# Performance work log

Measured on AMD Instinct MI355X. Metric: run time of the kernel, lower is better.

## Reference

```python
import jax, jax.numpy as jnp
import numpy as np

D = 512
H = 8
DH = D // H
FF = 2 * D
EPS = 1e-5


def _layernorm(x, g, b):
    mu = jnp.mean(x, axis=-1, keepdims=True)
    var = jnp.mean(jnp.square(x - mu), axis=-1, keepdims=True)
    return (x - mu) * jax.lax.rsqrt(var + EPS) * g + b


def setup_inputs() -> dict:
    key = jax.random.key(0)
    ks = jax.random.split(key, 8)
    s = 0.02
    x = jax.random.normal(ks[0], (1, 4096, D), dtype=jnp.float32)
    w_qkv = jax.random.normal(ks[1], (D, 3 * D), dtype=jnp.float32) * s
    b_qkv = jnp.zeros((3 * D,), jnp.float32)
    w_out = jax.random.normal(ks[2], (D, D), dtype=jnp.float32) * s
    b_out = jnp.zeros((D,), jnp.float32)
    w_ff1 = jax.random.normal(ks[3], (D, FF), dtype=jnp.float32) * s
    b_ff1 = jnp.zeros((FF,), jnp.float32)
    w_ff2 = jax.random.normal(ks[4], (FF, D), dtype=jnp.float32) * s
    b_ff2 = jnp.zeros((D,), jnp.float32)
    g1 = jnp.ones((D,), jnp.float32)
    bt1 = jnp.zeros((D,), jnp.float32)
    g2 = jnp.ones((D,), jnp.float32)
    bt2 = jnp.zeros((D,), jnp.float32)
    return {"x": x, "w_qkv": w_qkv, "b_qkv": b_qkv, "w_out": w_out, "b_out": b_out,
            "w_ff1": w_ff1, "b_ff1": b_ff1, "w_ff2": w_ff2, "b_ff2": b_ff2,
            "g1": g1, "bt1": bt1, "g2": g2, "bt2": bt2}


def reference(x, w_qkv, b_qkv, w_out, b_out, w_ff1, b_ff1, w_ff2, b_ff2, g1, bt1, g2, bt2):
    B, S, _ = x.shape
    h = _layernorm(x, g1, bt1)
    qkv = h @ w_qkv + b_qkv                      # [B,S,3D]
    qkv = qkv.reshape(B, S, 3, H, DH)
    q, k, v = qkv[:, :, 0], qkv[:, :, 1], qkv[:, :, 2]   # [B,S,H,DH]
    scores = jnp.einsum('bqhd,bkhd->bhqk', q, k) / np.sqrt(DH).astype(np.float32)
    causal = jnp.tril(jnp.ones((S, S), dtype=bool))
    scores = jnp.where(causal, scores, -jnp.inf)
    attn = jax.nn.softmax(scores, axis=-1)
    out = jnp.einsum('bhqk,bkhd->bqhd', attn, v).reshape(B, S, D)
    x = x + out @ w_out + b_out
    h2 = _layernorm(x, g2, bt2)
    ff = jax.nn.gelu(h2 @ w_ff1 + b_ff1, approximate=False) @ w_ff2 + b_ff2
    return x + ff
```

## Files before the change

kernel.cpp:

```cpp
#include <hip/hip_runtime.h>
#include <math.h>

#define D 512
#define H 8
#define DH 64
#define S 4096
#define FF 1024

typedef __attribute__((ext_vector_type(8))) short bf16x8;
typedef __attribute__((ext_vector_type(4))) float f32x4;
typedef __attribute__((ext_vector_type(16))) float f32x16;

__device__ __forceinline__ unsigned short f2bf(float f) {
    union { float f; unsigned u; } c; c.f = f;
    unsigned r = (c.u + 0x7fff + ((c.u >> 16) & 1)) >> 16;
    return (unsigned short)r;
}
__device__ __forceinline__ float bf2f(unsigned short u) {
    union { unsigned u; float f; } c; c.u = ((unsigned)u) << 16;
    return c.f;
}

__device__ __forceinline__ void gl_lds16(const void* g, void* l) {
    __builtin_amdgcn_global_load_lds(
        (const __attribute__((address_space(1))) void*)g,
        (__attribute__((address_space(3))) void*)l, 16, 0, 0);
}

__global__ __launch_bounds__(256) void transpose_all(const float* __restrict__ wqkv,
                                                     const float* __restrict__ wout,
                                                     const float* __restrict__ wff1,
                                                     const float* __restrict__ wff2,
                                                     unsigned short* __restrict__ oqkv,
                                                     unsigned short* __restrict__ oout,
                                                     unsigned short* __restrict__ off1,
                                                     unsigned short* __restrict__ off2) {
    __shared__ unsigned short tile[32][33];
    int id = blockIdx.x;
    const float* src; unsigned short* dst; int K, N, lid;
    if (id < 768)       { src = wqkv; dst = oqkv; K = 512;  N = 1536; lid = id; }
    else if (id < 1024) { src = wout; dst = oout; K = 512;  N = 512;  lid = id - 768; }
    else if (id < 1536) { src = wff1; dst = off1; K = 512;  N = 1024; lid = id - 1024; }
    else                { src = wff2; dst = off2; K = 1024; N = 512;  lid = id - 1536; }
    int nb = N / 32;
    int n0 = (lid % nb) * 32, k0 = (lid / nb) * 32;
    int tx = threadIdx.x & 31, ty = threadIdx.x >> 5;
#pragma unroll
    for (int i = 0; i < 32; i += 8)
        tile[ty + i][tx] = f2bf(src[(size_t)(k0 + ty + i) * N + n0 + tx]);
    __syncthreads();
#pragma unroll
    for (int i = 0; i < 32; i += 8)
        dst[(size_t)(n0 + ty + i) * K + k0 + tx] = tile[tx][ty + i];
}

__global__ __launch_bounds__(256) void transpose_v(const unsigned short* __restrict__ qkv,
                                                   unsigned short* __restrict__ vT) {
    __shared__ unsigned short tile[32][33];
    int s0 = blockIdx.x * 32, d0 = blockIdx.y * 32;
    int tx = threadIdx.x & 31, ty = threadIdx.x >> 5;
#pragma unroll
    for (int i = 0; i < 32; i += 8)
        tile[ty + i][tx] = qkv[(size_t)(s0 + ty + i) * (3 * D) + 2 * D + d0 + tx];
    __syncthreads();
#pragma unroll
    for (int i = 0; i < 32; i += 8)
        vT[(size_t)(d0 + ty + i) * S + s0 + tx] = tile[tx][ty + i];
}

__global__ __launch_bounds__(256) void ln_kernel(const float* __restrict__ x,
                                                 const float* __restrict__ g,
                                                 const float* __restrict__ bta,
                                                 unsigned short* __restrict__ out) {
    int row = blockIdx.x, tid = threadIdx.x;
    const float* xr = x + (size_t)row * D;
    float2 v = *(const float2*)(xr + tid * 2);
    float s = v.x + v.y;
    float sq = v.x * v.x + v.y * v.y;
#pragma unroll
    for (int m = 1; m < 64; m <<= 1) { s += __shfl_xor(s, m); sq += __shfl_xor(sq, m); }
    __shared__ float red[8];
    int wave = tid >> 6, lane = tid & 63;
    if (lane == 0) { red[wave] = s; red[4 + wave] = sq; }
    __syncthreads();
    s = red[0] + red[1] + red[2] + red[3];
    sq = red[4] + red[5] + red[6] + red[7];
    float mu = s * (1.f / D);
    float var = sq * (1.f / D) - mu * mu;
    float rstd = rsqrtf(var + 1e-5f);
    int i = tid * 2;
    float2 gg = *(const float2*)(g + i);
    float2 bb = *(const float2*)(bta + i);
    out[(size_t)row * D + i]     = f2bf((v.x - mu) * rstd * gg.x + bb.x);
    out[(size_t)row * D + i + 1] = f2bf((v.y - mu) * rstd * gg.y + bb.y);
}

enum { EPI_BF16 = 0, EPI_RESID_F32 = 1, EPI_GELU_BF16 = 2 };

template <int EPI, int WMI>
__global__ __launch_bounds__(256, WMI == 4 ? 2 : 3)
void gemm3_kernel(const unsigned short* __restrict__ A,
                  const unsigned short* __restrict__ BT,
                  const float* __restrict__ bias,
                  const float* __restrict__ resid,
                  void* __restrict__ out,
                  int M, int N, int K) {
    constexpr int BM = 32 * WMI;
    constexpr int BN = 128;
    constexpr int APH = BM * 8 / 256;
    __shared__ __align__(16) unsigned short sA[2][BM * 64];
    __shared__ __align__(16) unsigned short sB[2][BN * 64];

    int tid = threadIdx.x;
    int wave = tid >> 6, lane = tid & 63;
    int quad = lane >> 4, l16 = lane & 15;
    int lx = l16 & 7;
    int wr = (wave >> 1) * (BM / 2), wc = (wave & 1) * 64;
    int m0 = blockIdx.y * BM, n0 = blockIdx.x * BN;

    f32x4 acc[WMI][4];
#pragma unroll
    for (int i = 0; i < WMI; i++)
#pragma unroll
        for (int j = 0; j < 4; j++) acc[i][j] = (f32x4){0.f, 0.f, 0.f, 0.f};

    int srow = tid >> 3;
    int spc = tid & 7;
    int scc = spc ^ (srow & 7);
    const unsigned short* Abase = A + (size_t)(m0 + srow) * K + scc * 8;
    const unsigned short* Bbase = BT + (size_t)(n0 + srow) * K + scc * 8;
    int wofs = (tid & ~63) * 8;

    auto stage = [&](int k0, int buf) {
#pragma unroll
        for (int ph = 0; ph < APH; ph++)
            gl_lds16(Abase + (size_t)(ph * 32) * K + k0, sA[buf] + wofs + ph * 2048);
#pragma unroll
        for (int ph = 0; ph < 4; ph++)
            gl_lds16(Bbase + (size_t)(ph * 32) * K + k0, sB[buf] + wofs + ph * 2048);
    };

    int nk = K / 64;
    stage(0, 0);
    for (int ki = 0; ki < nk; ki++) {
        int buf = ki & 1;
        if (ki + 1 < nk) {
            stage((ki + 1) * 64, buf ^ 1);
            if constexpr (WMI == 4)
                asm volatile("s_waitcnt vmcnt(8)" ::: "memory");
            else
                asm volatile("s_waitcnt vmcnt(6)" ::: "memory");
        } else {
            asm volatile("s_waitcnt vmcnt(0)" ::: "memory");
        }
        __syncthreads();

#pragma unroll
        for (int ks = 0; ks < 2; ks++) {
            int cxs = ((ks * 4 + quad) ^ lx) * 8;
            bf16x8 af[WMI], bfr[4];
#pragma unroll
            for (int mi = 0; mi < WMI; mi++)
                af[mi] = *(const bf16x8*)(&sA[buf][(wr + mi * 16 + l16) * 64 + cxs]);
#pragma unroll
            for (int ni = 0; ni < 4; ni++)
                bfr[ni] = *(const bf16x8*)(&sB[buf][(wc + ni * 16 + l16) * 64 + cxs]);
#pragma unroll
            for (int mi = 0; mi < WMI; mi++)
#pragma unroll
                for (int ni = 0; ni < 4; ni++)
                    acc[mi][ni] = __builtin_amdgcn_mfma_f32_16x16x32_bf16(af[mi], bfr[ni], acc[mi][ni], 0, 0, 0);
        }
        __syncthreads();
    }

#pragma unroll
    for (int mi = 0; mi < WMI; mi++)
#pragma unroll
        for (int ni = 0; ni < 4; ni++) {
            int col = n0 + wc + ni * 16 + l16;
            float bs = bias[col];
#pragma unroll
            for (int r = 0; r < 4; r++) {
                int row = m0 + wr + mi * 16 + quad * 4 + r;
                float v = acc[mi][ni][r] + bs;
                size_t idx = (size_t)row * N + col;
                if constexpr (EPI == EPI_RESID_F32) {
                    ((float*)out)[idx] = v + resid[idx];
                } else if constexpr (EPI == EPI_GELU_BF16) {
                    v = 0.5f * v * (1.f + erff(v * 0.70710678118f));
                    ((unsigned short*)out)[idx] = f2bf(v);
                } else {
                    ((unsigned short*)out)[idx] = f2bf(v);
                }
            }
        }
}

#define LDO 68

__global__ __launch_bounds__(256, 4) void flash8_kernel(const unsigned short* __restrict__ qkv,
                                                        const unsigned short* __restrict__ vT,
                                                        unsigned short* __restrict__ O_part,
                                                        float* __restrict__ l_part) {
    __shared__ __align__(16) unsigned short sMem[4][64 * 64];

    int tid = threadIdx.x;
    int w = tid >> 6, lane = tid & 63;
    int lq = lane & 31, hb = lane >> 5;

    int h = blockIdx.x & 7;
    int u = blockIdx.x >> 3;
    int Q = 31, c = 0, acc = 0;
    for (int qq = 31; qq >= 0; --qq) {
        int n = (qq >> 2) + 1;
        if (u < acc + n) { Q = qq; c = u - acc; break; }
        acc += n;
    }
    int T = 2 * Q + 2;
    int t0c = c * 8;
    int t1c = min(t0c + 8, T);
    int q0w = Q * 128 + w * 32;
    int qrow = q0w + lq;
    int qmax = q0w + 31;

    const float CEXP = 0.18033688f;

    bf16x8 qf[4];
#pragma unroll
    for (int dc = 0; dc < 4; dc++)
        qf[dc] = *(const bf16x8*)(qkv + (size_t)qrow * (3 * D) + h * DH + dc * 16 + hb * 8);

    f32x16 oa[2];
#pragma unroll
    for (int i = 0; i < 16; i++) { oa[0][i] = 0.f; oa[1][i] = 0.f; }
    float l4[4] = {0.f, 0.f, 0.f, 0.f};

    int rr = tid >> 3;
    int spc = tid & 7;
    int scc = spc ^ (rr & 7);
    const unsigned short* kgb = qkv + (size_t)rr * (3 * D) + D + h * DH + scc * 8;
    const unsigned short* vgb = vT + (size_t)(h * DH + rr) * S + scc * 8;

    auto stage = [&](int t, int buf) {
        const unsigned short* kg = kgb + (size_t)t * 64 * (3 * D);
        const unsigned short* vg = vgb + t * 64;
        unsigned short* dK = sMem[buf] + w * 512;
        unsigned short* dV = sMem[2 + buf] + w * 512;
        gl_lds16(kg, dK);
        gl_lds16(kg + (size_t)32 * (3 * D), dK + 2048);
        gl_lds16(vg, dV);
        gl_lds16(vg + (size_t)32 * S, dV + 2048);
    };

    stage(t0c, 0);
    for (int t = t0c; t < t1c; ++t) {
        int buf = (t - t0c) & 1;
        asm volatile("s_waitcnt vmcnt(0)" ::: "memory");
        __syncthreads();
        if (t + 1 < t1c) stage(t + 1, buf ^ 1);

        if (64 * t > qmax) continue;

        f32x16 sa[2];
#pragma unroll
        for (int i = 0; i < 16; i++) { sa[0][i] = 0.f; sa[1][i] = 0.f; }
#pragma unroll
        for (int kt = 0; kt < 2; kt++)
#pragma unroll
            for (int dc = 0; dc < 4; dc++) {
                int ch = ((dc * 2 + hb) ^ (lq & 7)) * 8;
                bf16x8 kfr = *(const bf16x8*)(&sMem[buf][(kt * 32 + lq) * 64 + ch]);
                sa[kt] = __builtin_amdgcn_mfma_f32_32x32x16_bf16(kfr, qf[dc], sa[kt], 0, 0, 0);
            }

        bool dmask = (64 * t + 63 > qmax);
        unsigned p2[2][8];
        if (!dmask) {
#pragma unroll
            for (int kt = 0; kt < 2; kt++) {
                float e[16];
#pragma unroll
                for (int r = 0; r < 16; r++) {
                    e[r] = __builtin_amdgcn_exp2f(sa[kt][r] * CEXP);
                    l4[r & 3] += e[r];
                }
#pragma unroll
                for (int p = 0; p < 8; p++)
                    p2[kt][p] = ((unsigned)f2bf(e[2 * p + 1]) << 16) | f2bf(e[2 * p]);
            }
        } else {
#pragma unroll
            for (int kt = 0; kt < 2; kt++) {
                float e[16];
#pragma unroll
                for (int r = 0; r < 16; r++) {
                    float v = __builtin_amdgcn_exp2f(sa[kt][r] * CEXP);
                    int key = 64 * t + kt * 32 + (r & 3) + 8 * (r >> 2) + 4 * hb;
                    if (key > qrow) v = 0.f;
                    e[r] = v;
                    l4[r & 3] += v;
                }
#pragma unroll
                for (int p = 0; p < 8; p++)
                    p2[kt][p] = ((unsigned)f2bf(e[2 * p + 1]) << 16) | f2bf(e[2 * p]);
            }
        }

#pragma unroll
        for (int kc = 0; kc < 4; kc++) {
            int kt = kc >> 1;
            int b0i = (kc & 1) * 4;
            unsigned a0 = p2[kt][b0i + 0], a1 = p2[kt][b0i + 1];
            unsigned b0 = p2[kt][b0i + 2], b1 = p2[kt][b0i + 3];
            unsigned s0 = hb ? a0 : b0, s1 = hb ? a1 : b1;
            unsigned x0 = __shfl_xor(s0, 32), x1 = __shfl_xor(s1, 32);
            unsigned l0 = hb ? b0 : a0, l1 = hb ? b1 : a1;
            union { unsigned u[4]; bf16x8 v; } fr;
            fr.u[0] = hb ? x0 : l0;
            fr.u[1] = hb ? x1 : l1;
            fr.u[2] = hb ? l0 : x0;
            fr.u[3] = hb ? l1 : x1;
#pragma unroll
            for (int dt = 0; dt < 2; dt++) {
                int ch = ((kc * 2 + hb) ^ (lq & 7)) * 8;
                bf16x8 vfr = *(const bf16x8*)(&sMem[2 + buf][(dt * 32 + lq) * 64 + ch]);
                oa[dt] = __builtin_amdgcn_mfma_f32_32x32x16_bf16(vfr, fr.v, oa[dt], 0, 0, 0);
            }
        }
    }

    float lsum = (l4[0] + l4[1]) + (l4[2] + l4[3]);
    lsum += __shfl_xor(lsum, 32);
    if (hb == 0)
        l_part[((size_t)c * H + h) * S + q0w + lq] = lsum;

    __syncthreads();
    unsigned short* sOw = (unsigned short*)sMem + w * 32 * LDO;
#pragma unroll
    for (int kt = 0; kt < 2; kt++)
#pragma unroll
        for (int r = 0; r < 16; r++) {
            int d = kt * 32 + (r & 3) + 8 * (r >> 2) + 4 * hb;
            sOw[lq * LDO + d] = f2bf(oa[kt][r]);
        }
    asm volatile("s_waitcnt lgkmcnt(0)" ::: "memory");
    unsigned short* Op = O_part + ((size_t)c * S + q0w) * D + h * DH;
#pragma unroll
    for (int it = 0; it < 4; it++) {
        int rq = (lane >> 3) + it * 8;
        bf16x8 val = *(const bf16x8*)(sOw + rq * LDO + (lane & 7) * 8);
        *(bf16x8*)(Op + (size_t)rq * D + (lane & 7) * 8) = val;
    }
}

__global__ __launch_bounds__(256) void norm_kernel(const unsigned short* __restrict__ O_part,
                                                   const float* __restrict__ l_part,
                                                   unsigned short* __restrict__ O) {
    int idx = blockIdx.x * 256 + threadIdx.x;
    int row = idx >> 6;
    int c8 = (idx & 63) * 8;
    int h = c8 >> 6;
    int nch = ((row >> 7) >> 2) + 1;
    float o[8] = {0.f, 0.f, 0.f, 0.f, 0.f, 0.f, 0.f, 0.f};
    float l = 0.f;
    for (int cc = 0; cc < nch; cc++) {
        bf16x8 v = *(const bf16x8*)(O_part + ((size_t)cc * S + row) * D + c8);
#pragma unroll
        for (int j = 0; j < 8; j++) o[j] += bf2f((unsigned short)v[j]);
        l += l_part[((size_t)cc * H + h) * S + row];
    }
    float inv = 1.f / l;
    bf16x8 r;
#pragma unroll
    for (int j = 0; j < 8; j++) r[j] = (short)f2bf(o[j] * inv);
    *(bf16x8*)(O + (size_t)row * D + c8) = r;
}

extern "C" void kernel_launch(void* const* d_in, const int* in_sizes, int n_in,
                              void* d_out, int out_size, void* d_ws, size_t ws_size,
                              hipStream_t stream) {
    const float* x     = (const float*)d_in[0];
    const float* w_qkv = (const float*)d_in[1];
    const float* b_qkv = (const float*)d_in[2];
    const float* w_out = (const float*)d_in[3];
    const float* b_out = (const float*)d_in[4];
    const float* w_ff1 = (const float*)d_in[5];
    const float* b_ff1 = (const float*)d_in[6];
    const float* w_ff2 = (const float*)d_in[7];
    const float* b_ff2 = (const float*)d_in[8];
    const float* g1    = (const float*)d_in[9];
    const float* bt1   = (const float*)d_in[10];
    const float* g2    = (const float*)d_in[11];
    const float* bt2   = (const float*)d_in[12];

    char* ws = (char*)d_ws;
    size_t off = 0;
    auto alloc = [&](size_t bytes) {
        void* p = ws + off;
        off += (bytes + 255) & ~(size_t)255;
        return p;
    };
    unsigned short* hbuf   = (unsigned short*)alloc((size_t)S * D * 2);
    unsigned short* qkvbuf = (unsigned short*)alloc((size_t)S * 3 * D * 2);
    unsigned short* vTbuf  = (unsigned short*)alloc((size_t)D * S * 2);
    unsigned short* Obuf   = (unsigned short*)alloc((size_t)S * D * 2);
    unsigned short* wqkvT  = (unsigned short*)alloc((size_t)3 * D * D * 2);
    unsigned short* woutT  = (unsigned short*)alloc((size_t)D * D * 2);
    unsigned short* wff1T  = (unsigned short*)alloc((size_t)FF * D * 2);
    unsigned short* wff2T  = (unsigned short*)alloc((size_t)D * FF * 2);
    unsigned short* Opart  = (unsigned short*)alloc((size_t)8 * S * D * 2);
    float*          lpart  = (float*)alloc((size_t)8 * H * S * 4);
    unsigned short* h2buf  = hbuf;
    unsigned short* ff1buf = qkvbuf;
    float*          x2buf  = (float*)Opart;

    transpose_all<<<dim3(2048), 256, 0, stream>>>(w_qkv, w_out, w_ff1, w_ff2,
                                                  wqkvT, woutT, wff1T, wff2T);

    ln_kernel<<<S, 256, 0, stream>>>(x, g1, bt1, hbuf);
    gemm3_kernel<EPI_BF16, 4><<<dim3(12, 32), 256, 0, stream>>>(
        hbuf, wqkvT, b_qkv, nullptr, qkvbuf, S, 3 * D, D);
    transpose_v<<<dim3(S / 32, D / 32), 256, 0, stream>>>(qkvbuf, vTbuf);
    flash8_kernel<<<dim3(1152), 256, 0, stream>>>(qkvbuf, vTbuf, Opart, lpart);
    norm_kernel<<<dim3(S * D / 8 / 256), 256, 0, stream>>>(Opart, lpart, Obuf);
    gemm3_kernel<EPI_RESID_F32, 2><<<dim3(4, 64), 256, 0, stream>>>(
        Obuf, woutT, b_out, x, x2buf, S, D, D);
    ln_kernel<<<S, 256, 0, stream>>>(x2buf, g2, bt2, h2buf);
    gemm3_kernel<EPI_GELU_BF16, 4><<<dim3(8, 32), 256, 0, stream>>>(
        h2buf, wff1T, b_ff1, nullptr, ff1buf, S, FF, D);
    gemm3_kernel<EPI_RESID_F32, 2><<<dim3(4, 64), 256, 0, stream>>>(
        ff1buf, wff2T, b_ff2, x2buf, (float*)d_out, S, D, FF);
}
```

Measured before the change: 201.7 us.

## Fuse V transpose into QKV GEMM epilogue and triple-buffer flash K/V staging

The QKV GEMM epilogue now also writes the V columns transposed into vT as packed 4-element stores, which removes the separate transpose_v kernel launch and its re-read of qkv. The flash attention kernel goes from double to triple-buffered LDS K/V tiles. It issues the next tile's loads before waiting on the current one, with a partial vmcnt, so loads overlap compute. The extra LDS use lowers the occupancy hint from 4 to 3 blocks per CU, and the scattered vT stores may be poorly coalesced.

```diff
diff --git a/kernel.cpp b/kernel.cpp
--- a/kernel.cpp
+++ b/kernel.cpp
@@ -54,20 +54,6 @@
         dst[(size_t)(n0 + ty + i) * K + k0 + tx] = tile[tx][ty + i];
 }
 
-__global__ __launch_bounds__(256) void transpose_v(const unsigned short* __restrict__ qkv,
-                                                   unsigned short* __restrict__ vT) {
-    __shared__ unsigned short tile[32][33];
-    int s0 = blockIdx.x * 32, d0 = blockIdx.y * 32;
-    int tx = threadIdx.x & 31, ty = threadIdx.x >> 5;
-#pragma unroll
-    for (int i = 0; i < 32; i += 8)
-        tile[ty + i][tx] = qkv[(size_t)(s0 + ty + i) * (3 * D) + 2 * D + d0 + tx];
-    __syncthreads();
-#pragma unroll
-    for (int i = 0; i < 32; i += 8)
-        vT[(size_t)(d0 + ty + i) * S + s0 + tx] = tile[tx][ty + i];
-}
-
 __global__ __launch_bounds__(256) void ln_kernel(const float* __restrict__ x,
                                                  const float* __restrict__ g,
                                                  const float* __restrict__ bta,
@@ -97,13 +83,14 @@
 
 enum { EPI_BF16 = 0, EPI_RESID_F32 = 1, EPI_GELU_BF16 = 2 };
 
-template <int EPI, int WMI>
+template <int EPI, int WMI, bool QKV>
 __global__ __launch_bounds__(256, WMI == 4 ? 2 : 3)
 void gemm3_kernel(const unsigned short* __restrict__ A,
                   const unsigned short* __restrict__ BT,
                   const float* __restrict__ bias,
                   const float* __restrict__ resid,
                   void* __restrict__ out,
+                  unsigned short* __restrict__ vTout,
                   int M, int N, int K) {
     constexpr int BM = 32 * WMI;
     constexpr int BN = 128;
@@ -180,30 +167,41 @@
         for (int ni = 0; ni < 4; ni++) {
             int col = n0 + wc + ni * 16 + l16;
             float bs = bias[col];
+            int row0 = m0 + wr + mi * 16 + quad * 4;
+            unsigned short tv[4];
 #pragma unroll
             for (int r = 0; r < 4; r++) {
-                int row = m0 + wr + mi * 16 + quad * 4 + r;
                 float v = acc[mi][ni][r] + bs;
-                size_t idx = (size_t)row * N + col;
+                size_t idx = (size_t)(row0 + r) * N + col;
                 if constexpr (EPI == EPI_RESID_F32) {
                     ((float*)out)[idx] = v + resid[idx];
                 } else if constexpr (EPI == EPI_GELU_BF16) {
                     v = 0.5f * v * (1.f + erff(v * 0.70710678118f));
                     ((unsigned short*)out)[idx] = f2bf(v);
                 } else {
-                    ((unsigned short*)out)[idx] = f2bf(v);
+                    unsigned short b = f2bf(v);
+                    ((unsigned short*)out)[idx] = b;
+                    tv[r] = b;
                 }
             }
+            if constexpr (QKV) {
+                if (col >= 2 * D) {
+                    unsigned lo = (unsigned)tv[0] | ((unsigned)tv[1] << 16);
+                    unsigned hi = (unsigned)tv[2] | ((unsigned)tv[3] << 16);
+                    uint2 pk; pk.x = lo; pk.y = hi;
+                    *(uint2*)(vTout + (size_t)(col - 2 * D) * S + row0) = pk;
+                }
+            }
         }
 }
 
 #define LDO 68
 
-__global__ __launch_bounds__(256, 4) void flash8_kernel(const unsigned short* __restrict__ qkv,
+__global__ __launch_bounds__(256, 3) void flash9_kernel(const unsigned short* __restrict__ qkv,
                                                         const unsigned short* __restrict__ vT,
                                                         unsigned short* __restrict__ O_part,
                                                         float* __restrict__ l_part) {
-    __shared__ __align__(16) unsigned short sMem[4][64 * 64];
+    __shared__ __align__(16) unsigned short sMem[6][64 * 64];
 
     int tid = threadIdx.x;
     int w = tid >> 6, lane = tid & 63;
@@ -246,7 +244,7 @@
         const unsigned short* kg = kgb + (size_t)t * 64 * (3 * D);
         const unsigned short* vg = vgb + t * 64;
         unsigned short* dK = sMem[buf] + w * 512;
-        unsigned short* dV = sMem[2 + buf] + w * 512;
+        unsigned short* dV = sMem[3 + buf] + w * 512;
         gl_lds16(kg, dK);
         gl_lds16(kg + (size_t)32 * (3 * D), dK + 2048);
         gl_lds16(vg, dV);
@@ -255,10 +253,14 @@
 
     stage(t0c, 0);
     for (int t = t0c; t < t1c; ++t) {
-        int buf = (t - t0c) & 1;
-        asm volatile("s_waitcnt vmcnt(0)" ::: "memory");
+        int bufc = (t - t0c) % 3;
+        if (t + 1 < t1c) {
+            stage(t + 1, (t + 1 - t0c) % 3);
+            asm volatile("s_waitcnt vmcnt(4)" ::: "memory");
+        } else {
+            asm volatile("s_waitcnt vmcnt(0)" ::: "memory");
+        }
         __syncthreads();
-        if (t + 1 < t1c) stage(t + 1, buf ^ 1);
 
         if (64 * t > qmax) continue;
 
@@ -270,7 +272,7 @@
 #pragma unroll
             for (int dc = 0; dc < 4; dc++) {
                 int ch = ((dc * 2 + hb) ^ (lq & 7)) * 8;
-                bf16x8 kfr = *(const bf16x8*)(&sMem[buf][(kt * 32 + lq) * 64 + ch]);
+                bf16x8 kfr = *(const bf16x8*)(&sMem[bufc][(kt * 32 + lq) * 64 + ch]);
                 sa[kt] = __builtin_amdgcn_mfma_f32_32x32x16_bf16(kfr, qf[dc], sa[kt], 0, 0, 0);
             }
 
@@ -324,7 +326,7 @@
 #pragma unroll
             for (int dt = 0; dt < 2; dt++) {
                 int ch = ((kc * 2 + hb) ^ (lq & 7)) * 8;
-                bf16x8 vfr = *(const bf16x8*)(&sMem[2 + buf][(dt * 32 + lq) * 64 + ch]);
+                bf16x8 vfr = *(const bf16x8*)(&sMem[3 + bufc][(dt * 32 + lq) * 64 + ch]);
                 oa[dt] = __builtin_amdgcn_mfma_f32_32x32x16_bf16(vfr, fr.v, oa[dt], 0, 0, 0);
             }
         }
@@ -419,16 +421,15 @@
                                                   wqkvT, woutT, wff1T, wff2T);
 
     ln_kernel<<<S, 256, 0, stream>>>(x, g1, bt1, hbuf);
-    gemm3_kernel<EPI_BF16, 4><<<dim3(12, 32), 256, 0, stream>>>(
-        hbuf, wqkvT, b_qkv, nullptr, qkvbuf, S, 3 * D, D);
-    transpose_v<<<dim3(S / 32, D / 32), 256, 0, stream>>>(qkvbuf, vTbuf);
-    flash8_kernel<<<dim3(1152), 256, 0, stream>>>(qkvbuf, vTbuf, Opart, lpart);
+    gemm3_kernel<EPI_BF16, 4, true><<<dim3(12, 32), 256, 0, stream>>>(
+        hbuf, wqkvT, b_qkv, nullptr, qkvbuf, vTbuf, S, 3 * D, D);
+    flash9_kernel<<<dim3(1152), 256, 0, stream>>>(qkvbuf, vTbuf, Opart, lpart);
     norm_kernel<<<dim3(S * D / 8 / 256), 256, 0, stream>>>(Opart, lpart, Obuf);
-    gemm3_kernel<EPI_RESID_F32, 2><<<dim3(4, 64), 256, 0, stream>>>(
-        Obuf, woutT, b_out, x, x2buf, S, D, D);
+    gemm3_kernel<EPI_RESID_F32, 2, false><<<dim3(4, 64), 256, 0, stream>>>(
+        Obuf, woutT, b_out, x, x2buf, nullptr, S, D, D);
     ln_kernel<<<S, 256, 0, stream>>>(x2buf, g2, bt2, h2buf);
-    gemm3_kernel<EPI_GELU_BF16, 4><<<dim3(8, 32), 256, 0, stream>>>(
-        h2buf, wff1T, b_ff1, nullptr, ff1buf, S, FF, D);
-    gemm3_kernel<EPI_RESID_F32, 2><<<dim3(4, 64), 256, 0, stream>>>(
-        ff1buf, wff2T, b_ff2, x2buf, (float*)d_out, S, D, FF);
-}
+    gemm3_kernel<EPI_GELU_BF16, 4, false><<<dim3(8, 32), 256, 0, stream>>>(
+        h2buf, wff1T, b_ff1, nullptr, ff1buf, nullptr, S, FF, D);
+    gemm3_kernel<EPI_RESID_F32, 2, false><<<dim3(4, 64), 256, 0, stream>>>(
+        ff1buf, wff2T, b_ff2, x2buf, (float*)d_out, nullptr, S, D, FF);
+}
```

New measurement: 197.3 us. -2.2%, faster.
